# Kernel tuning notes

Measured on AMD Instinct MI355X. Metric: run time of the kernel, lower is better.

Reference implementation:

```python
import jax, jax.numpy as jnp
import numpy as np

G = 64          # number of global tokens (first G positions are global)
NUM_HEADS = 16
WINDOW = 512    # attention_window (one-sided w = 256)


def _chunk(x, w):
    # x: [BH, S, D] -> overlapping chunks of size 2w with overlap w
    BH, S, D = x.shape
    f = x.reshape(BH, S // w, w, D)
    return jnp.concatenate([f[:, :-1], f[:, 1:]], axis=2)  # [BH, S//w-1, 2w, D]


def _mask_invalid(x, w):
    # x: [B, S, H, 2w+1]; -inf at out-of-sequence window positions
    B, S, H, W = x.shape
    m = jnp.flip(jnp.tril(jnp.ones((w, w + 1), x.dtype)), axis=0)
    m = jnp.pad(m, ((0, S - w), (0, W - w - 1)))
    m = m + jnp.flip(m, axis=(0, 1))
    return jnp.where((m > 0)[None, :, None, :], -jnp.inf, x)


def _sliding_qk(q, k, w):
    # q, k: [B, S, H, D] -> banded scores [B, S, H, 2w+1]
    B, S, H, D = q.shape
    C = S // w - 1
    qf = q.transpose(0, 2, 1, 3).reshape(B * H, S, D)
    kf = k.transpose(0, 2, 1, 3).reshape(B * H, S, D)
    s = jnp.einsum('bcxd,bcyd->bcxy', _chunk(qf, w), _chunk(kf, w))  # [BH,C,2w,2w]
    diag = jnp.pad(s, ((0, 0), (0, 0), (0, 1), (0, 0))).transpose(0, 1, 3, 2)  # [BH,C,2w,2w+1]
    up = jnp.concatenate([diag[:, :, :w, :w + 1], diag[:, -1:, w:, :w + 1]], axis=1)
    z = jnp.zeros((B * H, 1, w, w), diag.dtype)
    low = jnp.concatenate([z, diag[:, :, -(w + 1):-1, w + 1:]], axis=1)
    first = jnp.concatenate([jnp.roll(diag, shift=(1, w), axis=(2, 3))[:, :, :w, :w], z], axis=1)
    low = jnp.where(jnp.arange(C + 1)[None, :, None, None] < 1, first, low)
    full = jnp.concatenate([low, up], axis=-1).reshape(B, H, S, 2 * w + 1).transpose(0, 2, 1, 3)
    return _mask_invalid(full, w)


def _sliding_pv(probs, v, w):
    # probs: [B, S, H, 2w+1], v: [B, S, H, D] -> [B, S, H, D]
    B, S, H, _ = probs.shape
    D = v.shape[-1]
    nc = S // w
    p = probs.transpose(0, 2, 1, 3).reshape(B * H, nc, w, 2 * w + 1)
    vf = v.transpose(0, 2, 1, 3).reshape(B * H, S, D)
    pv = jnp.pad(vf, ((0, 0), (w, w), (0, 0)), constant_values=-1.0)
    idx = jnp.arange(nc)[:, None] * w + jnp.arange(3 * w)[None, :]
    cv = pv[:, idx]  # [BH, nc, 3w, D]
    # pad-and-diagonalize the banded probs into [w, 3w]
    pd = jnp.pad(p, ((0, 0), (0, 0), (0, 0), (0, w + 1)))
    pd = pd.reshape(B * H, nc, w * (3 * w + 2))[:, :, :-w]
    pd = pd.reshape(B * H, nc, w, 3 * w + 1)[:, :, :, :-1]  # [BH,nc,w,3w]
    out = jnp.einsum('bcwd,bcdh->bcwh', pd, cv)
    return out.reshape(B, H, S, D).transpose(0, 2, 1, 3)


def _forward(hidden_states, attention_mask, Wq, bq, Wk, bk, Wv, bv,
             Wqg, bqg, Wkg, bkg, Wvg, bvg, is_index_masked, is_index_global_attn):
    B, S, E = hidden_states.shape
    H = NUM_HEADS
    D = E // H
    w = WINDOW // 2
    q = (hidden_states @ Wq + bq) / jnp.sqrt(jnp.float32(D))
    k = hidden_states @ Wk + bk
    v = hidden_states @ Wv + bv
    q4 = q.reshape(B, S, H, D)
    k4 = k.reshape(B, S, H, D)
    v4 = v.reshape(B, S, H, D)
    local = _sliding_qk(q4, k4, w)                         # [B,S,H,2w+1]
    diag_mask = _sliding_qk(jnp.ones_like(attention_mask), attention_mask, w)  # [B,S,1,2w+1]
    local = local + diag_mask
    # global key columns (first G tokens global) prepended to the band
    g_scores = jnp.einsum('bshd,bghd->bshg', q4, k4[:, :G])
    scores = jnp.concatenate([g_scores, local], axis=-1)   # [B,S,H,G+2w+1]
    probs = jax.nn.softmax(scores, axis=-1)
    probs = jnp.where(is_index_masked[:, :, None, None], 0.0, probs)
    out_g = jnp.einsum('bshg,bghd->bshd', probs[..., :G], v4[:, :G])
    out_l = _sliding_pv(probs[..., G:], v4, w)
    attn_output = (out_g + out_l).reshape(B, S, E)
    # global tokens attend to the full sequence with the *_global projections
    qg = ((hidden_states[:, :G] @ Wqg + bqg) / jnp.sqrt(jnp.float32(D))).reshape(B, G, H, D).transpose(0, 2, 1, 3)
    kg = (hidden_states @ Wkg + bkg).reshape(B, S, H, D).transpose(0, 2, 1, 3)
    vg = (hidden_states @ Wvg + bvg).reshape(B, S, H, D).transpose(0, 2, 1, 3)
    gs = jnp.einsum('bhgd,bhsd->bhgs', qg, kg)             # [B,H,G,S]
    gs = jnp.where(is_index_masked[:, None, None, :], -10000.0, gs)
    gp = jax.nn.softmax(gs, axis=-1)
    go = jnp.einsum('bhgs,bhsd->bhgd', gp, vg).transpose(0, 2, 1, 3).reshape(B, G, E)
    attn_output = attn_output.at[:, :G].set(go)            # scatter global rows
    probs = jnp.where(is_index_global_attn[:, :, None, None], 0.0, probs)
    return attn_output, probs, gp


def setup_inputs() -> dict:
    key = jax.random.key(0)
    B, S, E = 2, 4096, 1024
    ks = jax.random.split(key, 8)
    std = 0.02
    d = lambda k: std * jax.random.normal(k, (E, E), jnp.float32)
    zb = jnp.zeros((E,), jnp.float32)
    return {
        'hidden_states': jax.random.normal(ks[0], (B, S, E), jnp.float32),
        'attention_mask': jnp.zeros((B, S, 1, 1), jnp.float32),
        'Wq': d(ks[1]), 'bq': zb, 'Wk': d(ks[2]), 'bk': zb, 'Wv': d(ks[3]), 'bv': zb,
        'Wqg': d(ks[4]), 'bqg': zb, 'Wkg': d(ks[5]), 'bkg': zb, 'Wvg': d(ks[6]), 'bvg': zb,
        'is_index_masked': jnp.zeros((B, S), bool),
        'is_index_global_attn': jnp.broadcast_to(jnp.arange(S)[None, :] < G, (B, S)),
        'is_global_attn': 1,
    }


def reference(hidden_states, attention_mask, Wq, bq, Wk, bk, Wv, bv,
              Wqg, bqg, Wkg, bkg, Wvg, bvg,
              is_index_masked, is_index_global_attn, is_global_attn):
    # is_global_attn is statically 1 (global path always taken)
    return _forward(hidden_states, attention_mask, Wq, bq, Wk, bk, Wv, bv,
                    Wqg, bqg, Wkg, bkg, Wvg, bvg, is_index_masked, is_index_global_attn)
```

## Files before the change

### kernel.cpp

```cpp
#include <hip/hip_runtime.h>
#include <hip/hip_bf16.h>
#include <cstdint>
#include <cstddef>

typedef short s16x8 __attribute__((ext_vector_type(8)));
typedef float f32x4 __attribute__((ext_vector_type(4)));

#define DEV static __device__ __forceinline__

DEV unsigned short f2bf(float x){
  union { float f; unsigned int u; } v; v.f = x;
  unsigned int u = v.u;
  return (unsigned short)((u + 0x7FFFu + ((u >> 16) & 1u)) >> 16);
}
DEV float bf2f(unsigned short b){
  union { unsigned int u; float f; } v; v.u = ((unsigned int)b) << 16;
  return v.f;
}
DEV void ntst(float* p, float v){ __builtin_nontemporal_store(v, p); }

DEV void bar_lgkm(){
  asm volatile("s_waitcnt lgkmcnt(0)" ::: "memory");
  __builtin_amdgcn_s_barrier();
  __builtin_amdgcn_sched_barrier(0);
}

DEV void gld16(unsigned short* lds, const unsigned short* g){
  __builtin_amdgcn_global_load_lds(
      (const __attribute__((address_space(1))) void*)g,
      (__attribute__((address_space(3))) void*)lds, 16, 0, 0);
}

__global__ __launch_bounds__(256) void cast_x(const float* __restrict__ X,
                                              unsigned short* __restrict__ out,
                                              unsigned short* __restrict__ Xg){
  int i = (blockIdx.x*256 + threadIdx.x)*4;
  float4 v = *(const float4*)(X + i);
  ushort4 r;
  r.x = f2bf(v.x); r.y = f2bf(v.y); r.z = f2bf(v.z); r.w = f2bf(v.w);
  *(ushort4*)(out + i) = r;
  int row = i >> 10;
  int s = row & 4095, b = row >> 12;
  if (s < 64)
    *(ushort4*)(Xg + (size_t)(b*64 + s)*1024 + (i & 1023)) = r;
}

__global__ __launch_bounds__(256) void bias_cat_k(
    const float* bq, const float* bk, const float* bv,
    const float* bkg, const float* bvg, const float* bqg,
    float* __restrict__ bc, float* __restrict__ bqg_o){
  int i = blockIdx.x*256 + threadIdx.x;
  if (i < 5120){
    int slot = i >> 10, c = i & 1023;
    const float* s = (slot==0)?bq:(slot==1)?bk:(slot==2)?bv:(slot==3)?bkg:bvg;
    bc[i] = s[c];
  } else {
    bqg_o[i-5120] = bqg[i-5120];
  }
}

struct WSrc { const float* p[6]; };

__global__ __launch_bounds__(256) void wt_transpose(WSrc srcs,
    unsigned short* __restrict__ Wtcat, unsigned short* __restrict__ Wtqg){
  __shared__ float t[64*66];
  int bi = blockIdx.x;
  int widx = bi >> 8;
  int tile = bi & 255;
  int tn = tile & 15, tk = tile >> 4;
  int k0 = tk*64, n0 = tn*64;
  const float* W = srcs.p[widx];
  int tid = threadIdx.x;
  for (int it=0; it<8; ++it){
    int flat = it*256 + tid;
    int r = flat >> 5, ch = flat & 31;
    *(float2*)&t[r*66 + ch*2] = *(const float2*)(W + (size_t)(k0+r)*1024 + n0 + ch*2);
  }
  __syncthreads();
  unsigned short* dst = (widx==3) ? Wtqg
                      : Wtcat + (size_t)((widx<3)?widx:widx-1)*1048576;
  for (int it=0; it<16; ++it){
    int flat = it*256 + tid;
    int i = flat >> 6, j = flat & 63;
    dst[(size_t)(n0+i)*1024 + k0 + j] = f2bf(t[j*66 + i]);
  }
}

#define G8_LDS 131072
__global__ __launch_bounds__(512) void gemm8(
    const unsigned short* __restrict__ A, const unsigned short* __restrict__ Bt,
    const float* __restrict__ bias, unsigned short* __restrict__ C,
    int Astr, int Bstr, int Cstr, int scale_cols)
{
  extern __shared__ unsigned short lds[];
  int tid = threadIdx.x, lane = tid & 63, wv = tid >> 6;
  int wr = wv >> 2, wc = wv & 3;
  int lane15 = lane & 15, kh = (lane >> 4) << 3;
  int m0 = blockIdx.y*256, n0 = blockIdx.x*256;

  f32x4 acc[8][4];
#pragma unroll
  for (int i=0;i<8;i++)
#pragma unroll
    for (int j=0;j<4;j++) acc[i][j] = (f32x4){0.f,0.f,0.f,0.f};

#pragma unroll
  for (int ht=0; ht<4; ++ht){
    int ktn = ht>>1, half = ht&1;
    unsigned short* sA = lds + (ht&3)*16384;
    unsigned short* sB = sA + 8192;
#pragma unroll
    for (int cc=0; cc<2; ++cc){
      int c = cc*512 + tid, r = c>>3, ch = c&7;
      int co = ktn*64 + ((ch ^ (r&7))<<3);
      gld16(sA + c*8, A  + (size_t)(m0 + half*128 + r)*Astr + co);
      gld16(sB + c*8, Bt + (size_t)(n0 + half*128 + r)*Bstr + co);
    }
  }
  asm volatile("s_waitcnt vmcnt(8)" ::: "memory");
  __builtin_amdgcn_s_barrier();
  __builtin_amdgcn_sched_barrier(0);

  for (int kt = 0; kt < 16; ++kt){
    unsigned short* aslot = lds + ((2*kt + wr)&3)*16384;
    unsigned short* bslot = lds + ((2*kt + (wc>>1))&3)*16384 + 8192;
    s16x8 bfr[4][2];
#pragma unroll
    for (int n=0;n<4;n++){
      int r = (wc&1)*64 + n*16 + lane15;
#pragma unroll
      for (int ks=0;ks<2;ks++)
        bfr[n][ks] = *(const s16x8*)&bslot[(r<<6) + ((ks*32 + kh) ^ ((r&7)<<3))];
    }
    __builtin_amdgcn_s_setprio(1);
#pragma unroll
    for (int m=0;m<8;m++){
      int r = m*16 + lane15;
      s16x8 a0 = *(const s16x8*)&aslot[(r<<6) + (kh ^ ((r&7)<<3))];
      s16x8 a1 = *(const s16x8*)&aslot[(r<<6) + ((32 + kh) ^ ((r&7)<<3))];
#pragma unroll
      for (int n=0;n<4;n++){
        acc[m][n] = __builtin_amdgcn_mfma_f32_16x16x32_bf16(a0, bfr[n][0], acc[m][n], 0,0,0);
        acc[m][n] = __builtin_amdgcn_mfma_f32_16x16x32_bf16(a1, bfr[n][1], acc[m][n], 0,0,0);
      }
    }
    __builtin_amdgcn_s_setprio(0);
    bar_lgkm();
    if (kt < 14){
#pragma unroll
      for (int hh=0; hh<2; ++hh){
        int ht = 2*kt + 4 + hh;
        int ktn = ht>>1, half = ht&1;
        unsigned short* sA = lds + (ht&3)*16384;
        unsigned short* sB = sA + 8192;
#pragma unroll
        for (int cc=0; cc<2; ++cc){
          int c = cc*512 + tid, r = c>>3, ch = c&7;
          int co = ktn*64 + ((ch ^ (r&7))<<3);
          gld16(sA + c*8, A  + (size_t)(m0 + half*128 + r)*Astr + co);
          gld16(sB + c*8, Bt + (size_t)(n0 + half*128 + r)*Bstr + co);
        }
      }
      asm volatile("s_waitcnt vmcnt(8)" ::: "memory");
    } else {
      asm volatile("s_waitcnt vmcnt(0)" ::: "memory");
    }
    __builtin_amdgcn_s_barrier();
    __builtin_amdgcn_sched_barrier(0);
  }

#pragma unroll
  for (int m=0;m<8;m++){
    int mb = m0 + wr*128 + m*16 + ((lane>>4)<<2);
#pragma unroll
    for (int n=0;n<4;n++){
      int col = n0 + wc*64 + n*16 + lane15;
      float bb = bias[col];
      float sc = (col < scale_cols) ? 0.125f : 1.0f;
#pragma unroll
      for (int r=0;r<4;r++)
        C[(size_t)(mb+r)*Cstr + col] = f2bf((acc[m][n][r] + bb)*sc);
    }
  }
}

__global__ __launch_bounds__(256) void gemm_bt(
    const unsigned short* __restrict__ A, const unsigned short* __restrict__ Bt,
    const float* __restrict__ bias, unsigned short* __restrict__ C,
    int Astr, int Bstr, int Cstr, int scale_cols)
{
  __shared__ unsigned short lA[128*64];
  __shared__ unsigned short lB[128*64];
  int tid = threadIdx.x, lane = tid & 63, wv = tid >> 6;
  int wm = wv >> 1, wn = wv & 1;
  int lane15 = lane & 15, kh = (lane >> 4) << 3;
  int m0 = blockIdx.y*128, n0 = blockIdx.x*128;
  f32x4 acc[4][4];
  for (int i=0;i<4;i++) for (int j=0;j<4;j++) acc[i][j] = (f32x4){0.f,0.f,0.f,0.f};
  for (int k0 = 0; k0 < 1024; k0 += 64){
#pragma unroll
    for (int it = 0; it < 4; ++it){
      int chunk = it*256 + tid;
      int r = chunk >> 3, ch = chunk & 7;
      int co = ((ch ^ (r & 7)) << 3);
      gld16(&lA[chunk*8], A  + (size_t)(m0+r)*Astr + k0 + co);
      gld16(&lB[chunk*8], Bt + (size_t)(n0+r)*Bstr + k0 + co);
    }
    __syncthreads();
#pragma unroll
    for (int ks = 0; ks < 2; ++ks){
      s16x8 af[4], bfr[4];
#pragma unroll
      for (int i=0;i<4;i++){
        int row = wm*64 + i*16 + lane15;
        af[i] = *(const s16x8*)&lA[(row<<6) + ((ks*32 + kh) ^ ((row&7)<<3))];
      }
#pragma unroll
      for (int j=0;j<4;j++){
        int row = wn*64 + j*16 + lane15;
        bfr[j] = *(const s16x8*)&lB[(row<<6) + ((ks*32 + kh) ^ ((row&7)<<3))];
      }
#pragma unroll
      for (int i=0;i<4;i++)
#pragma unroll
        for (int j=0;j<4;j++)
          acc[i][j] = __builtin_amdgcn_mfma_f32_16x16x32_bf16(af[i], bfr[j], acc[i][j], 0,0,0);
    }
    __syncthreads();
  }
  for (int i=0;i<4;i++){
    int mb = m0 + wm*64 + i*16 + ((lane>>4)<<2);
    for (int j=0;j<4;j++){
      int n = n0 + wn*64 + j*16 + lane15;
      float bb = bias[n];
      float sc = (n < scale_cols) ? 0.125f : 1.0f;
#pragma unroll
      for (int r=0;r<4;r++)
        C[(size_t)(mb+r)*Cstr + n] = f2bf((acc[i][j][r] + bb)*sc);
    }
  }
}

__global__ __launch_bounds__(256) void vt_transpose(
    const unsigned short* __restrict__ proj, unsigned short* __restrict__ dst,
    int coloff){
  __shared__ unsigned short t[64*72];
  int bi = blockIdx.x;
  int sc = bi & 63, h = (bi>>6) & 15, b = bi >> 10;
  int s0 = sc*64;
  int tid = threadIdx.x;
  for (int it=0; it<2; ++it){
    int flat = it*256 + tid;
    int r = flat >> 3, ch = flat & 7;
    *(int4*)&t[r*72 + ch*8] =
      *(const int4*)(proj + (size_t)(b*4096+s0+r)*5120 + coloff + h*64 + ch*8);
  }
  __syncthreads();
  for (int it=0; it<2; ++it){
    int flat = it*256 + tid;
    int d = flat & 63, ch = flat >> 6;
    unsigned short tmp[8];
#pragma unroll
    for (int j=0;j<8;j++) tmp[j] = t[(ch*8+j)*72 + d];
    *(int4*)(dst + ((size_t)(b*16+h)*64 + d)*4096 + s0 + ch*8) = *(int4*)tmp;
  }
}

#define SSTR 612
__global__ __launch_bounds__(512) void sliding_attn(
    const unsigned short* __restrict__ proj,
    const unsigned short* __restrict__ vt,
    const float* __restrict__ amask,
    const unsigned char* __restrict__ maskb,
    float* __restrict__ probs,
    float* __restrict__ attn)
{
  __shared__ float sS[16*SSTR];
  __shared__ float srs[16];
  int bi = (blockIdx.x & 7)*1024 + (blockIdx.x >> 3);
  int ti = bi & 255, h = (bi>>8) & 15, b = bi >> 12;
  int t = ti*16;
  int chk = t >> 8;
  int qu = (chk < 15) ? chk*256 : 3584;
  int ql = (chk >= 1) ? chk*256 : 256;
  int tid = threadIdx.x, lane = tid & 63, wv = tid >> 6;
  int lane15 = lane & 15, kh = (lane >> 4) << 3;
  int rbase = (lane>>4)<<2;

  s16x8 aq0 = {}, aq1 = {}, ak0a = {}, ak0b = {}, ak1a = {}, ak1b = {};
  {
    int qrow = t + lane15;
    if (wv == 0){
      const unsigned short* qp = proj + (size_t)(b*4096+qrow)*5120 + h*64 + kh;
      aq0 = *(const s16x8*)qp;  aq1 = *(const s16x8*)(qp + 32);
    }
    if (wv >= 4){
      const unsigned short* kp0 = proj + (size_t)(b*4096+qrow)*5120 + 1024 + h*64 + kh;
      ak0a = *(const s16x8*)kp0; ak0b = *(const s16x8*)(kp0 + 32);
    }
    if (wv <= 3){
      int krow = t - 1 + lane15; if (krow < 0) krow = 0;
      const unsigned short* kp1 = proj + (size_t)(b*4096+krow)*5120 + 1024 + h*64 + kh;
      ak1a = *(const s16x8*)kp1; ak1b = *(const s16x8*)(kp1 + 32);
    }
  }

  {
    int ct0 = wv*5;
#pragma unroll
    for (int j5 = 0; j5 < 5; ++j5){
      int ct = ct0 + j5;
      if (ct < 37){
        int col = ct*16 + lane15;
        int brow, roff;
        if (ct < 4){        brow = col;               roff = 1024; }
        else if (ct < 20){  brow = ql + 1 + col - 64; roff = 0;
                            if (brow > 4095) brow = 4095; }
        else {              brow = qu + col - 320;    roff = 0; }
        const unsigned short* bp = proj + (size_t)(b*4096+brow)*5120 + roff + h*64 + kh;
        s16x8 b0 = *(const s16x8*)bp;
        s16x8 b1 = *(const s16x8*)(bp + 32);
        s16x8 A0 = (ct<4) ? aq0 : (ct<20) ? ak1a : ak0a;
        s16x8 A1 = (ct<4) ? aq1 : (ct<20) ? ak1b : ak0b;
        f32x4 acc = (f32x4){0.f,0.f,0.f,0.f};
        __builtin_amdgcn_s_setprio(1);
        acc = __builtin_amdgcn_mfma_f32_16x16x32_bf16(A0, b0, acc, 0,0,0);
        acc = __builtin_amdgcn_mfma_f32_16x16x32_bf16(A1, b1, acc, 0,0,0);
        __builtin_amdgcn_s_setprio(0);
        if (col <= 576){
          int sk = (ct >= 4);
#pragma unroll
          for (int r=0;r<4;r++){
            int row = rbase + r;
            sS[row*SSTR + col + (sk ? row : 0)] = acc[r];
          }
        }
      }
    }
  }

  int dg = wv & 3, khalf = wv >> 2;
  int dcol = dg*16 + lane15;
  const unsigned short* vtb = vt + ((size_t)(b*16+h)*64 + dcol)*4096;
  int kc0 = khalf*10, kcn = khalf ? 9 : 10;
  s16x8 vB[10];
#pragma unroll
  for (int j = 0; j < 10; ++j){
    if (j < kcn){
      int kk = (kc0 + j)*32 + kh;
      int key = (kk < 64) ? kk : (t - 320 + kk);
      key = key < 0 ? 0 : (key > 4088 ? 4088 : key);
      vB[j] = *(const s16x8*)(vtb + key);
    }
  }

  bar_lgkm();

  {
    int r0 = wv*2;
    float low_add[2], up_add[2];
#pragma unroll
    for (int rr=0;rr<2;rr++){
      int s = t + r0 + rr;
      low_add[rr] = (s >= 1) ? amask[b*4096 + s - 1] : 0.f;
      up_add[rr]  = amask[b*4096 + s];
    }
    float ereg[2][10];
    float sum4[2] = {0.f,0.f};
#pragma unroll
    for (int i=0;i<10;i++){
      int c = lane + i*64;
      bool inr = (c < 577);
      bool isup = (c >= 320), islow = (c >= 64) & !isup;
      int jup = c - 320, jlow = c - 64;
#pragma unroll
      for (int rr=0;rr<2;rr++){
        int r = r0 + rr;
        float e = 0.f;
        if (inr){
          float v = sS[r*SSTR + c + ((c>=64) ? r : 0)];
          int ii = (t + r) & 255;
          if (isup){
            bool valid = !((chk==15) & (jup >= 256 - ii));
            v = valid ? v + up_add[rr] : -1e30f;
          } else if (islow){
            bool valid = !((chk==0) & (jlow < 256 - ii));
            v = valid ? ((jlow==255) ? 0.f : v + low_add[rr]) : -1e30f;
          }
          e = __expf(v);
          ((unsigned short*)&sS[r*SSTR])[c + ((c>=64) ? r : 0)] = f2bf(e);
        }
        ereg[rr][i] = e;
        sum4[rr] += e;
      }
    }
#pragma unroll
    for (int o=32;o;o>>=1){
#pragma unroll
      for (int rr=0;rr<2;rr++) sum4[rr] += __shfl_xor(sum4[rr], o);
    }
#pragma unroll
    for (int rr=0;rr<2;rr++){
      int r = r0 + rr, s = t + r;
      float rs = 1.f / sum4[rr];
      float mz = maskb[b*4096 + s] ? 0.f : 1.f;
      float pz = (s < 64) ? 0.f : mz;
      float* prow = probs + ((size_t)(b*4096+s)*16 + h)*577;
#pragma unroll
      for (int i=0;i<10;i++){
        int c = lane + i*64;
        if (c < 577) ntst(prow + c, ereg[rr][i] * rs * pz);
      }
      if (lane < 31){
        int zc = (lane < r) ? 64 + lane : 577 + lane;
        ((unsigned short*)&sS[r*SSTR])[zc] = 0;
      }
      if (lane == 0) srs[r] = rs * mz;
    }
  }
  bar_lgkm();

  const unsigned short* prow16 = (const unsigned short*)(sS + (size_t)lane15*SSTR);
  f32x4 oacc = (f32x4){0.f,0.f,0.f,0.f};
  __builtin_amdgcn_s_setprio(1);
#pragma unroll
  for (int j = 0; j < 10; ++j){
    if (j < kcn){
      s16x8 ap = *(const s16x8*)(prow16 + (kc0 + j)*32 + kh);
      oacc = __builtin_amdgcn_mfma_f32_16x16x32_bf16(ap, vB[j], oacc, 0,0,0);
    }
  }
  __builtin_amdgcn_s_setprio(0);
  if (khalf == 1){
#pragma unroll
    for (int r=0;r<4;r++){
      int flat = dg*256 + (rbase + r)*16 + lane15;
      sS[(flat>>8)*SSTR + 336 + (flat & 255)] = oacc[r];
    }
  }
  bar_lgkm();
  if (khalf == 0){
#pragma unroll
    for (int r=0;r<4;r++){
      int flat = dg*256 + (rbase + r)*16 + lane15;
      float part = sS[(flat>>8)*SSTR + 336 + (flat & 255)];
      ntst(attn + (size_t)(b*4096 + t + rbase + r)*1024 + h*64 + dcol,
           (oacc[r] + part) * srs[rbase + r]);
    }
  }
}

__global__ __launch_bounds__(256) void gs_a2(
    const unsigned short* __restrict__ qg,
    const unsigned short* __restrict__ proj,
    const unsigned char* __restrict__ maskb,
    float* __restrict__ gp)
{
  __shared__ unsigned short sQ[64*68];
  int bi = blockIdx.x;
  int sc = bi & 15, h = (bi>>4) & 15, b = bi >> 8;
  int tid = threadIdx.x, lane = tid & 63, wv = tid >> 6;
  int lane15 = lane & 15, kh = (lane >> 4) << 3;
#pragma unroll
  for (int it=0; it<2; ++it){
    int flat = it*256 + tid;
    int g = flat >> 3, ch = (flat & 7) << 3;
    *(s16x8*)&sQ[g*68 + ch] = *(const s16x8*)(qg + (size_t)(b*64+g)*1024 + h*64 + ch);
  }
  __syncthreads();
  s16x8 a[4][2];
#pragma unroll
  for (int gt=0; gt<4; ++gt)
#pragma unroll
    for (int ks=0; ks<2; ++ks)
      a[gt][ks] = *(const s16x8*)&sQ[(gt*16+lane15)*68 + ks*32 + kh];
  int s0 = sc*256 + wv*64;
  float* gpb_ = gp + (size_t)(b*16+h)*64*4096;
#pragma unroll
  for (int st=0; st<4; ++st){
    int s = s0 + st*16 + lane15;
    const unsigned short* kp = proj + (size_t)(b*4096+s)*5120 + 3072 + h*64 + kh;
    s16x8 b0 = *(const s16x8*)kp;
    s16x8 b1 = *(const s16x8*)(kp + 32);
    bool msk = maskb[b*4096 + s] != 0;
    f32x4 acc[4];
#pragma unroll
    for (int gt=0; gt<4; ++gt){
      acc[gt] = (f32x4){0.f,0.f,0.f,0.f};
      acc[gt] = __builtin_amdgcn_mfma_f32_16x16x32_bf16(a[gt][0], b0, acc[gt], 0,0,0);
      acc[gt] = __builtin_amdgcn_mfma_f32_16x16x32_bf16(a[gt][1], b1, acc[gt], 0,0,0);
    }
#pragma unroll
    for (int gt=0; gt<4; ++gt){
#pragma unroll
      for (int r=0;r<4;r++){
        int g = gt*16 + (lane>>4)*4 + r;
        ntst(gpb_ + (size_t)g*4096 + s, msk ? -10000.f : acc[gt][r]);
      }
    }
  }
}

__global__ __launch_bounds__(256) void gs_norm(float* __restrict__ gp,
                                               unsigned short* __restrict__ gpb){
  __shared__ float red[8];
  int bi = blockIdx.x;
  float* row = gp + (size_t)bi*4096;
  int tid = threadIdx.x, lane = tid & 63, wv = tid >> 6;
  float v[16];
  float m = -1e30f;
#pragma unroll
  for (int i=0;i<16;i++){
    v[i] = row[tid + i*256];
    m = fmaxf(m, v[i]);
  }
#pragma unroll
  for (int o=32;o;o>>=1) m = fmaxf(m, __shfl_xor(m, o));
  if (!lane) red[wv] = m;
  __syncthreads();
  m = fmaxf(fmaxf(red[0],red[1]), fmaxf(red[2],red[3]));
  float s = 0.f;
#pragma unroll
  for (int i=0;i<16;i++){
    float e = __expf(v[i] - m);
    v[i] = e;
    s += e;
  }
#pragma unroll
  for (int o=32;o;o>>=1) s += __shfl_xor(s, o);
  if (!lane) red[4+wv] = s;
  __syncthreads();
  s = red[4]+red[5]+red[6]+red[7];
  float rs = 1.f / s;
#pragma unroll
  for (int i=0;i<16;i++){
    float p = v[i] * rs;
    ntst(row + tid + i*256, p);
    gpb[(size_t)bi*4096 + tid + i*256] = f2bf(p);
  }
}

__global__ __launch_bounds__(256) void go_mfma(
    const unsigned short* __restrict__ gpb,
    const unsigned short* __restrict__ vgt,
    float* __restrict__ gop)
{
  int bi = blockIdx.x;
  int kc = bi & 7, bh = bi >> 3;
  int tid = threadIdx.x, lane = tid & 63, wv = tid >> 6;
  int lane15 = lane & 15, kh = (lane >> 4) << 3;
  const unsigned short* arow = gpb + ((size_t)bh*64 + wv*16 + lane15)*4096 + kh;
  const unsigned short* bbase = vgt + (size_t)bh*64*4096 + kh;
  f32x4 acc[4];
#pragma unroll
  for (int j=0;j<4;j++) acc[j] = (f32x4){0.f,0.f,0.f,0.f};
  for (int ks = 0; ks < 16; ++ks){
    int k = kc*512 + ks*32;
    s16x8 a = *(const s16x8*)(arow + k);
#pragma unroll
    for (int j=0;j<4;j++){
      s16x8 bv = *(const s16x8*)(bbase + (size_t)(j*16 + lane15)*4096 + k);
      acc[j] = __builtin_amdgcn_mfma_f32_16x16x32_bf16(a, bv, acc[j], 0,0,0);
    }
  }
  int rq = (lane >> 4) << 2;
  float* o = gop + ((size_t)bh*8 + kc)*4096;
#pragma unroll
  for (int j=0;j<4;j++)
#pragma unroll
    for (int r=0;r<4;r++)
      o[(wv*16 + rq + r)*64 + j*16 + lane15] = acc[j][r];
}

__global__ __launch_bounds__(256) void reduce_go2(
    const float* __restrict__ gop, float* __restrict__ attn){
  int flat = blockIdx.x*256 + threadIdx.x;
  int gd = flat & 4095, bh = flat >> 12;
  int b = bh >> 4, h = bh & 15;
  int g = gd >> 6, d = gd & 63;
  const float* p = gop + (size_t)bh*8*4096 + gd;
  float sum = 0.f;
#pragma unroll
  for (int c=0; c<8; ++c) sum += p[c*4096];
  attn[(size_t)(b*4096 + g)*1024 + h*64 + d] = sum;
}

extern "C" void kernel_launch(void* const* d_in, const int* in_sizes, int n_in,
                              void* d_out, int out_size, void* d_ws, size_t ws_size,
                              hipStream_t stream)
{
  const float* X     = (const float*)d_in[0];
  const float* amask = (const float*)d_in[1];
  const float* Wq  = (const float*)d_in[2];  const float* bq  = (const float*)d_in[3];
  const float* Wk  = (const float*)d_in[4];  const float* bk  = (const float*)d_in[5];
  const float* Wv  = (const float*)d_in[6];  const float* bv  = (const float*)d_in[7];
  const float* Wqg = (const float*)d_in[8];  const float* bqg = (const float*)d_in[9];
  const float* Wkg = (const float*)d_in[10]; const float* bkg = (const float*)d_in[11];
  const float* Wvg = (const float*)d_in[12]; const float* bvg = (const float*)d_in[13];
  const unsigned char* imask = (const unsigned char*)d_in[14];
  (void)in_sizes; (void)n_in; (void)out_size;

  const size_t XBF  = 0;
  const size_t XG   = 16777216;
  const size_t WT   = 17039360;
  const size_t WTQG = 27525120;
  const size_t BC   = 29622272;
  const size_t BQG  = 29642752;
  const size_t PROJ = 29646848;
  const size_t QGO  = 113532928;
  const size_t VT   = 113795072;
  const size_t NEED = 130572288;
  if (ws_size < NEED) return;

  char* ws = (char*)d_ws;
  unsigned short* Xbf   = (unsigned short*)(ws + XBF);
  unsigned short* Xg    = (unsigned short*)(ws + XG);
  unsigned short* Wtcat = (unsigned short*)(ws + WT);
  unsigned short* Wtqg  = (unsigned short*)(ws + WTQG);
  float*          bc    = (float*)(ws + BC);
  float*          bqgo  = (float*)(ws + BQG);
  unsigned short* proj  = (unsigned short*)(ws + PROJ);
  unsigned short* qgo   = (unsigned short*)(ws + QGO);
  unsigned short* vt    = (unsigned short*)(ws + VT);
  unsigned short* gpb   = (unsigned short*)(ws + XBF);
  float*          gop   = (float*)(ws + WT);

  float* attn  = (float*)d_out;
  float* probs = (float*)d_out + 8388608;
  float* gp    = (float*)d_out + 84017152;

  hipFuncSetAttribute((const void*)gemm8,
                      hipFuncAttributeMaxDynamicSharedMemorySize, G8_LDS);

  cast_x<<<8192, 256, 0, stream>>>(X, Xbf, Xg);
  bias_cat_k<<<24, 256, 0, stream>>>(bq, bk, bv, bkg, bvg, bqg, bc, bqgo);
  WSrc srcs; srcs.p[0]=Wq; srcs.p[1]=Wk; srcs.p[2]=Wv; srcs.p[3]=Wqg; srcs.p[4]=Wkg; srcs.p[5]=Wvg;
  wt_transpose<<<1536, 256, 0, stream>>>(srcs, Wtcat, Wtqg);
  gemm8<<<dim3(20,32), 512, G8_LDS, stream>>>(Xbf, Wtcat, bc, proj, 1024, 1024, 5120, 1024);
  gemm_bt<<<dim3(8,1), 256, 0, stream>>>(Xg, Wtqg, bqgo, qgo, 1024, 1024, 1024, 1024);
  vt_transpose<<<2048, 256, 0, stream>>>(proj, vt, 2048);
  sliding_attn<<<8192, 512, 0, stream>>>(proj, vt, amask, imask, probs, attn);
  vt_transpose<<<2048, 256, 0, stream>>>(proj, vt, 4096);
  gs_a2<<<512, 256, 0, stream>>>(qgo, proj, imask, gp);
  gs_norm<<<2048, 256, 0, stream>>>(gp, gpb);
  go_mfma<<<256, 256, 0, stream>>>(gpb, vt, gop);
  reduce_go2<<<512, 256, 0, stream>>>(gop, attn);
}
```

Baseline: 374.0 us.

## Fuse V transpose into projection GEMM epilogue and split-K the global-query GEMM

The projection GEMM epilogue now also writes the local V columns transposed into the vt buffer with 8-byte nontemporal stores, which removes the first vt_transpose launch and its re-read of proj. The small global-query GEMM, which previously ran on only 8 blocks, is split over K into 32 blocks that write fp32 partials, followed by a reduce kernel that applies the bias and scaling. This raises parallelism for the tiny GEMM at the cost of an extra launch and partial-buffer traffic. The transposed V stores are strided and may be poorly coalesced.

```diff
diff --git a/kernel.cpp b/kernel.cpp
--- a/kernel.cpp
+++ b/kernel.cpp
@@ -18,6 +18,9 @@
   return v.f;
 }
 DEV void ntst(float* p, float v){ __builtin_nontemporal_store(v, p); }
+DEV void ntst8(void* p, unsigned long long v){
+  __builtin_nontemporal_store(v, (unsigned long long*)p);
+}
 
 DEV void bar_lgkm(){
   asm volatile("s_waitcnt lgkmcnt(0)" ::: "memory");
@@ -90,6 +93,7 @@
 __global__ __launch_bounds__(512) void gemm8(
     const unsigned short* __restrict__ A, const unsigned short* __restrict__ Bt,
     const float* __restrict__ bias, unsigned short* __restrict__ C,
+    unsigned short* __restrict__ vtv,
     int Astr, int Bstr, int Cstr, int scale_cols)
 {
   extern __shared__ unsigned short lds[];
@@ -177,66 +181,21 @@
       int col = n0 + wc*64 + n*16 + lane15;
       float bb = bias[col];
       float sc = (col < scale_cols) ? 0.125f : 1.0f;
-#pragma unroll
-      for (int r=0;r<4;r++)
-        C[(size_t)(mb+r)*Cstr + col] = f2bf((acc[m][n][r] + bb)*sc);
-    }
-  }
-}
-
-__global__ __launch_bounds__(256) void gemm_bt(
-    const unsigned short* __restrict__ A, const unsigned short* __restrict__ Bt,
-    const float* __restrict__ bias, unsigned short* __restrict__ C,
-    int Astr, int Bstr, int Cstr, int scale_cols)
-{
-  __shared__ unsigned short lA[128*64];
-  __shared__ unsigned short lB[128*64];
-  int tid = threadIdx.x, lane = tid & 63, wv = tid >> 6;
-  int wm = wv >> 1, wn = wv & 1;
-  int lane15 = lane & 15, kh = (lane >> 4) << 3;
-  int m0 = blockIdx.y*128, n0 = blockIdx.x*128;
-  f32x4 acc[4][4];
-  for (int i=0;i<4;i++) for (int j=0;j<4;j++) acc[i][j] = (f32x4){0.f,0.f,0.f,0.f};
-  for (int k0 = 0; k0 < 1024; k0 += 64){
-#pragma unroll
-    for (int it = 0; it < 4; ++it){
-      int chunk = it*256 + tid;
-      int r = chunk >> 3, ch = chunk & 7;
-      int co = ((ch ^ (r & 7)) << 3);
-      gld16(&lA[chunk*8], A  + (size_t)(m0+r)*Astr + k0 + co);
-      gld16(&lB[chunk*8], Bt + (size_t)(n0+r)*Bstr + k0 + co);
-    }
-    __syncthreads();
-#pragma unroll
-    for (int ks = 0; ks < 2; ++ks){
-      s16x8 af[4], bfr[4];
-#pragma unroll
-      for (int i=0;i<4;i++){
-        int row = wm*64 + i*16 + lane15;
-        af[i] = *(const s16x8*)&lA[(row<<6) + ((ks*32 + kh) ^ ((row&7)<<3))];
-      }
-#pragma unroll
-      for (int j=0;j<4;j++){
-        int row = wn*64 + j*16 + lane15;
-        bfr[j] = *(const s16x8*)&lB[(row<<6) + ((ks*32 + kh) ^ ((row&7)<<3))];
-      }
-#pragma unroll
-      for (int i=0;i<4;i++)
-#pragma unroll
-        for (int j=0;j<4;j++)
-          acc[i][j] = __builtin_amdgcn_mfma_f32_16x16x32_bf16(af[i], bfr[j], acc[i][j], 0,0,0);
-    }
-    __syncthreads();
-  }
-  for (int i=0;i<4;i++){
-    int mb = m0 + wm*64 + i*16 + ((lane>>4)<<2);
-    for (int j=0;j<4;j++){
-      int n = n0 + wn*64 + j*16 + lane15;
-      float bb = bias[n];
-      float sc = (n < scale_cols) ? 0.125f : 1.0f;
-#pragma unroll
-      for (int r=0;r<4;r++)
-        C[(size_t)(mb+r)*Cstr + n] = f2bf((acc[i][j][r] + bb)*sc);
+      unsigned short t4[4];
+#pragma unroll
+      for (int r=0;r<4;r++){
+        unsigned short bv = f2bf((acc[m][n][r] + bb)*sc);
+        t4[r] = bv;
+        C[(size_t)(mb+r)*Cstr + col] = bv;
+      }
+      if (col >= 2048 && col < 3072){
+        int cz = col - 2048;
+        int h = cz >> 6, d = cz & 63;
+        int b2 = mb >> 12, ss = mb & 4095;
+        unsigned long long pack;
+        __builtin_memcpy(&pack, t4, 8);
+        ntst8(vtv + (((size_t)(b2*16 + h)*64 + d)*4096 + ss), pack);
+      }
     }
   }
 }
@@ -264,6 +223,69 @@
     for (int j=0;j<8;j++) tmp[j] = t[(ch*8+j)*72 + d];
     *(int4*)(dst + ((size_t)(b*16+h)*64 + d)*4096 + s0 + ch*8) = *(int4*)tmp;
   }
+}
+
+__global__ __launch_bounds__(256) void gemm_qg(
+    const unsigned short* __restrict__ A, const unsigned short* __restrict__ Bt,
+    float* __restrict__ part)
+{
+  __shared__ unsigned short lA[128*64];
+  __shared__ unsigned short lB[128*64];
+  int tid = threadIdx.x, lane = tid & 63, wv = tid >> 6;
+  int wm = wv >> 1, wn = wv & 1;
+  int lane15 = lane & 15, kh = (lane >> 4) << 3;
+  int n0 = blockIdx.x*128, kb = blockIdx.y;
+  f32x4 acc[4][4];
+  for (int i=0;i<4;i++) for (int j=0;j<4;j++) acc[i][j] = (f32x4){0.f,0.f,0.f,0.f};
+  for (int k0 = kb*256; k0 < kb*256 + 256; k0 += 64){
+#pragma unroll
+    for (int it = 0; it < 4; ++it){
+      int chunk = it*256 + tid;
+      int r = chunk >> 3, ch = chunk & 7;
+      int co = ((ch ^ (r & 7)) << 3);
+      gld16(&lA[chunk*8], A  + (size_t)r*1024 + k0 + co);
+      gld16(&lB[chunk*8], Bt + (size_t)(n0+r)*1024 + k0 + co);
+    }
+    __syncthreads();
+#pragma unroll
+    for (int ks = 0; ks < 2; ++ks){
+      s16x8 af[4], bfr[4];
+#pragma unroll
+      for (int i=0;i<4;i++){
+        int row = wm*64 + i*16 + lane15;
+        af[i] = *(const s16x8*)&lA[(row<<6) + ((ks*32 + kh) ^ ((row&7)<<3))];
+      }
+#pragma unroll
+      for (int j=0;j<4;j++){
+        int row = wn*64 + j*16 + lane15;
+        bfr[j] = *(const s16x8*)&lB[(row<<6) + ((ks*32 + kh) ^ ((row&7)<<3))];
+      }
+#pragma unroll
+      for (int i=0;i<4;i++)
+#pragma unroll
+        for (int j=0;j<4;j++)
+          acc[i][j] = __builtin_amdgcn_mfma_f32_16x16x32_bf16(af[i], bfr[j], acc[i][j], 0,0,0);
+    }
+    __syncthreads();
+  }
+  float* o = part + (size_t)kb*131072;
+  for (int i=0;i<4;i++){
+    int mb = wm*64 + i*16 + ((lane>>4)<<2);
+    for (int j=0;j<4;j++){
+      int n = n0 + wn*64 + j*16 + lane15;
+#pragma unroll
+      for (int r=0;r<4;r++)
+        ntst(o + (size_t)(mb+r)*1024 + n, acc[i][j][r]);
+    }
+  }
+}
+
+__global__ __launch_bounds__(256) void reduce_qg(
+    const float* __restrict__ part, const float* __restrict__ bqg,
+    unsigned short* __restrict__ qgo){
+  int i = blockIdx.x*256 + threadIdx.x;
+  float s = part[i] + part[131072 + i] + part[262144 + i] + part[393216 + i];
+  qgo[i] = f2bf((s + bqg[i & 1023]) * 0.125f);
 }
 
 #define SSTR 612
@@ -624,6 +646,7 @@
   unsigned short* vt    = (unsigned short*)(ws + VT);
   unsigned short* gpb   = (unsigned short*)(ws + XBF);
   float*          gop   = (float*)(ws + WT);
+  float*          qgp   = (float*)(ws + WT + 4194304);
 
   float* attn  = (float*)d_out;
   float* probs = (float*)d_out + 8388608;
@@ -636,9 +659,10 @@
   bias_cat_k<<<24, 256, 0, stream>>>(bq, bk, bv, bkg, bvg, bqg, bc, bqgo);
   WSrc srcs; srcs.p[0]=Wq; srcs.p[1]=Wk; srcs.p[2]=Wv; srcs.p[3]=Wqg; srcs.p[4]=Wkg; srcs.p[5]=Wvg;
   wt_transpose<<<1536, 256, 0, stream>>>(srcs, Wtcat, Wtqg);
-  gemm8<<<dim3(20,32), 512, G8_LDS, stream>>>(Xbf, Wtcat, bc, proj, 1024, 1024, 5120, 1024);
-  gemm_bt<<<dim3(8,1), 256, 0, stream>>>(Xg, Wtqg, bqgo, qgo, 1024, 1024, 1024, 1024);
-  vt_transpose<<<2048, 256, 0, stream>>>(proj, vt, 2048);
+  gemm8<<<dim3(20,32), 512, G8_LDS, stream>>>(Xbf, Wtcat, bc, proj, vt,
+                                              1024, 1024, 5120, 1024);
+  gemm_qg<<<dim3(8,4), 256, 0, stream>>>(Xg, Wtqg, qgp);
+  reduce_qg<<<512, 256, 0, stream>>>(qgp, bqgo, qgo);
   sliding_attn<<<8192, 512, 0, stream>>>(proj, vt, amask, imask, probs, attn);
   vt_transpose<<<2048, 256, 0, stream>>>(proj, vt, 4096);
   gs_a2<<<512, 256, 0, stream>>>(qgo, proj, imask, gp);
```

New measurement: 378.8 us. No clear change (+1.3%).
